# Kernel optimization log

Hardware: AMD Instinct MI355X
Metric: run time of the kernel (lower is better)

## Reference

```python
import jax, jax.numpy as jnp
import numpy as np

B, S, D_IN, D_OUT, H = 2, 2048, 1024, 1024, 16
HD = D_OUT // H


def setup_inputs() -> dict:
    key = jax.random.key(0)
    ks = jax.random.split(key, 6)
    s = 0.02
    return {
        "X": jax.random.normal(ks[0], (B, S, D_IN), dtype=jnp.float32),
        "Wq": jax.random.normal(ks[1], (D_OUT, D_IN), dtype=jnp.float32) * s,
        "Wk": jax.random.normal(ks[2], (D_OUT, D_IN), dtype=jnp.float32) * s,
        "Wv": jax.random.normal(ks[3], (D_OUT, D_IN), dtype=jnp.float32) * s,
        "Wo": jax.random.normal(ks[4], (D_OUT, D_OUT), dtype=jnp.float32) * s,
        "bo": jax.random.normal(ks[5], (D_OUT,), dtype=jnp.float32) * s,
    }


def reference(X, Wq, Wk, Wv, Wo, bo):
    b, n, _ = X.shape
    # torch Linear: y = x @ W^T
    Q = (X @ Wq.T).reshape(b, n, H, HD).transpose(0, 2, 1, 3)  # [b,h,s,hd]
    K = (X @ Wk.T).reshape(b, n, H, HD).transpose(0, 2, 1, 3)
    V = (X @ Wv.T).reshape(b, n, H, HD).transpose(0, 2, 1, 3)
    S_ = jnp.einsum('bhqd,bhkd->bhqk', Q, K)  # [b,h,s,s]
    causal = jnp.triu(jnp.ones((n, n), dtype=bool), k=1)
    S_ = jnp.where(causal, -jnp.inf, S_)
    W = jax.nn.softmax(S_ / jnp.sqrt(jnp.float32(HD)), axis=-1)
    Z = jnp.einsum('bhqk,bhkd->bhqd', W, V)
    Z = Z.transpose(0, 2, 1, 3).reshape(b, n, D_OUT)
    return Z @ Wo.T + bo
```

## Files before the change

kernel.cpp:

```cpp
#include <hip/hip_runtime.h>
#include <stdint.h>

typedef __bf16 bf16x8 __attribute__((ext_vector_type(8)));
typedef float  f32x4  __attribute__((ext_vector_type(4)));

#define S_   2048
#define DM   1024
#define QSCALE 0.18033688011112042f

__device__ __forceinline__ unsigned short f2b(float f) {
    uint32_t u = __builtin_bit_cast(uint32_t, f);
    u += 0x7fffu + ((u >> 16) & 1u);
    return (unsigned short)(u >> 16);
}

__device__ __forceinline__ uint32_t pack2bf(float a, float b) {
    uint32_t ua = __builtin_bit_cast(uint32_t, a) + 0x8000u;
    uint32_t ub = __builtin_bit_cast(uint32_t, b) + 0x8000u;
    return __builtin_amdgcn_perm(ub, ua, 0x07060302);
}

__device__ __forceinline__ void glds16(const void* g, void* l) {
    __builtin_amdgcn_global_load_lds(
        (const __attribute__((address_space(1))) void*)g,
        (__attribute__((address_space(3))) void*)l, 16, 0, 0);
}

__global__ void cvt_all(const float* __restrict__ X,
                        const float* __restrict__ Wq, const float* __restrict__ Wk,
                        const float* __restrict__ Wv,
                        unsigned short* __restrict__ Xb, unsigned short* __restrict__ Wb)
{
    size_t i = ((size_t)blockIdx.x * 256 + threadIdx.x) * 4;
    const float* src;
    unsigned short* dst;
    size_t off;
    if (i < (size_t)4194304) { src = X; dst = Xb; off = i; }
    else {
        size_t j = i - 4194304;
        int sel = (int)(j >> 20);
        off = j & 1048575;
        src = (sel == 0) ? Wq : (sel == 1) ? Wk : Wv;
        dst = Wb + (size_t)sel * 1048576;
    }
    float4 v = *(const float4*)&src[off];
    uint2 o;
    o.x = pack2bf(v.x, v.y);
    o.y = pack2bf(v.z, v.w);
    *(uint2*)&dst[off] = o;
}

__global__ void cvt_wo(const float* __restrict__ Wo, unsigned short* __restrict__ Wob)
{
    size_t i = ((size_t)blockIdx.x * 256 + threadIdx.x) * 4;
    float4 v = *(const float4*)&Wo[i];
    uint2 o;
    o.x = pack2bf(v.x, v.y);
    o.y = pack2bf(v.z, v.w);
    *(uint2*)&Wob[i] = o;
}

__global__ __launch_bounds__(256, 2)
void qkv_gemm(const unsigned short* __restrict__ Xb,
              const unsigned short* __restrict__ Wqb,
              const unsigned short* __restrict__ Wkb,
              const unsigned short* __restrict__ Wvb,
              unsigned short* __restrict__ Qo, unsigned short* __restrict__ Ko,
              unsigned short* __restrict__ Vto)
{
    __shared__ unsigned short Ash[128 * 32];
    __shared__ unsigned short Bsh[128 * 32];

    const int t = threadIdx.x;
    const int lane = t & 63, w = t >> 6;
    const int lcol = lane & 15, quad = lane >> 4;
    const int z = blockIdx.z;
    const int rowBase = ((z == 2) ? blockIdx.x : blockIdx.y) * 128;
    const int colBase = ((z == 2) ? blockIdx.y : blockIdx.x) * 128;
    const unsigned short* aPtr = (z == 2) ? Wvb : Xb;
    const unsigned short* bPtr = (z == 0) ? Wqb : (z == 1) ? Wkb : Xb;
    const int wr = (w >> 1) * 64, wc = (w & 1) * 64;

    f32x4 acc[4][4];
    #pragma unroll
    for (int i = 0; i < 4; ++i)
        #pragma unroll
        for (int j = 0; j < 4; ++j) acc[i][j] = (f32x4){0.f,0.f,0.f,0.f};

    for (int k0 = 0; k0 < DM; k0 += 32) {
        __syncthreads();
        #pragma unroll
        for (int p = 0; p < 2; ++p) {
            int ci = p * 256 + t;
            glds16(&aPtr[(size_t)(rowBase + (ci >> 2)) * DM + k0 + (ci & 3) * 8], &Ash[ci * 8]);
        }
        #pragma unroll
        for (int p = 0; p < 2; ++p) {
            int ci = p * 256 + t;
            glds16(&bPtr[(size_t)(colBase + (ci >> 2)) * DM + k0 + (ci & 3) * 8], &Bsh[ci * 8]);
        }
        __syncthreads();
        bf16x8 af[4], bfr[4];
        #pragma unroll
        for (int i = 0; i < 4; ++i) af[i]  = *(const bf16x8*)&Ash[(wr + i*16 + lcol)*32 + quad*8];
        #pragma unroll
        for (int i = 0; i < 4; ++i) bfr[i] = *(const bf16x8*)&Bsh[(wc + i*16 + lcol)*32 + quad*8];
        #pragma unroll
        for (int i = 0; i < 4; ++i)
            #pragma unroll
            for (int j = 0; j < 4; ++j)
                acc[i][j] = __builtin_amdgcn_mfma_f32_16x16x32_bf16(af[i], bfr[j], acc[i][j], 0, 0, 0);
    }

    unsigned short* Cm = (z == 0) ? Qo : (z == 1) ? Ko : Vto;
    const int ld = (z == 2) ? (S_ * 2) : DM;
    const float sc = (z == 0) ? QSCALE : 1.0f;
    #pragma unroll
    for (int i = 0; i < 4; ++i)
        #pragma unroll
        for (int j = 0; j < 4; ++j)
            #pragma unroll
            for (int r = 0; r < 4; ++r) {
                int row = rowBase + wr + i*16 + quad*4 + r;
                int col = colBase + wc + j*16 + lcol;
                Cm[(size_t)row * ld + col] = f2b(acc[i][j][r] * sc);
            }
}

__global__ __launch_bounds__(512, 8)
void attn_kernel(const unsigned short* __restrict__ Q,
                 const unsigned short* __restrict__ K,
                 const unsigned short* __restrict__ Vt,
                 unsigned short* __restrict__ Z)
{
    __shared__ unsigned short Ks[64 * 72];
    __shared__ unsigned short Vts[64 * 72];
    __shared__ unsigned short Ps[128 * 72];

    const int t = threadIdx.x;
    const int lane = t & 63, w = t >> 6;
    const int lcol = lane & 15, quad = lane >> 4;

    const int bh = blockIdx.x;
    const int b = bh >> 4, h = bh & 15;
    const int y = blockIdx.y;
    const int tile = (y < 8) ? (15 - y) : (y - 8);
    const int q0 = tile * 128;
    const int nchunk = 2 * tile + 2;

    const unsigned short* Qg = Q + (size_t)(b * S_ + q0) * DM + h * 64;
    const unsigned short* Kg = K + (size_t)(b * S_) * DM + h * 64;
    const unsigned short* Vg = Vt + (size_t)(h * 64) * (S_ * 2) + b * S_;

    bf16x8 qf[2];
    #pragma unroll
    for (int kd = 0; kd < 2; ++kd)
        qf[kd] = *(const bf16x8*)&Qg[(size_t)(w*16 + lcol) * DM + kd*32 + quad*8];

    bool mk[4];
    #pragma unroll
    for (int r = 0; r < 4; ++r) mk[r] = (quad*4 + r) > lcol;

    float lpart = 0.f;
    f32x4 o[4];
    #pragma unroll
    for (int nd = 0; nd < 4; ++nd) o[nd] = (f32x4){0.f,0.f,0.f,0.f};

    const int sr = t >> 3, sch = t & 7;

    for (int c = 0; c < nchunk; ++c) {
        const int kc = c * 64;
        __syncthreads();
        *(uint4*)&Ks[sr * 72 + sch * 8] =
            *(const uint4*)&Kg[(size_t)(kc + sr) * DM + sch * 8];
        *(uint4*)&Vts[sr * 72 + sch * 8] =
            *(const uint4*)&Vg[(size_t)sr * (S_ * 2) + kc + sch * 8];
        __syncthreads();

        const int m = tile * 8 + w - c * 4;
        const int nkmax = (m >= 3) ? 4 : (m + 1);
        const int kdmax = (nkmax + 1) >> 1;

        #pragma unroll
        for (int nk = 0; nk < 4; ++nk) {
            if (nk < nkmax) {
                f32x4 s = (f32x4){0.f,0.f,0.f,0.f};
                bf16x8 ak0 = *(const bf16x8*)&Ks[(nk*16 + lcol)*72 + quad*8];
                s = __builtin_amdgcn_mfma_f32_16x16x32_bf16(ak0, qf[0], s, 0, 0, 0);
                bf16x8 ak1 = *(const bf16x8*)&Ks[(nk*16 + lcol)*72 + 32 + quad*8];
                s = __builtin_amdgcn_mfma_f32_16x16x32_bf16(ak1, qf[1], s, 0, 0, 0);
                float p0 = __builtin_amdgcn_exp2f(s[0]);
                float p1 = __builtin_amdgcn_exp2f(s[1]);
                float p2 = __builtin_amdgcn_exp2f(s[2]);
                float p3 = __builtin_amdgcn_exp2f(s[3]);
                if (nk == m) {
                    p0 = mk[0] ? 0.f : p0;
                    p1 = mk[1] ? 0.f : p1;
                    p2 = mk[2] ? 0.f : p2;
                    p3 = mk[3] ? 0.f : p3;
                }
                lpart += (p0 + p1) + (p2 + p3);
                uint2 pk;
                pk.x = pack2bf(p0, p1);
                pk.y = pack2bf(p2, p3);
                *(uint2*)&Ps[(w*16 + lcol) * 72 + nk*16 + quad*4] = pk;
            } else if (nk < 2*kdmax) {
                *(uint2*)&Ps[(w*16 + lcol) * 72 + nk*16 + quad*4] = (uint2){0u, 0u};
            }
        }

        #pragma unroll
        for (int kd2 = 0; kd2 < 2; ++kd2) {
            if (kd2 < kdmax) {
                bf16x8 ap = *(const bf16x8*)&Ps[(w*16 + lcol) * 72 + kd2*32 + quad*8];
                #pragma unroll
                for (int nd = 0; nd < 4; ++nd) {
                    bf16x8 bv = *(const bf16x8*)&Vts[(nd*16 + lcol) * 72 + kd2*32 + quad*8];
                    o[nd] = __builtin_amdgcn_mfma_f32_16x16x32_bf16(ap, bv, o[nd], 0, 0, 0);
                }
            }
        }
    }

    lpart += __shfl_xor(lpart, 16);
    lpart += __shfl_xor(lpart, 32);
    float linv = 1.0f / lpart;
    #pragma unroll
    for (int r = 0; r < 4; ++r) {
        float lr = __shfl(linv, quad*4 + r);
        unsigned short* Zr = Z + (size_t)(b*S_ + q0 + w*16 + quad*4 + r) * DM + h*64;
        #pragma unroll
        for (int nd = 0; nd < 4; ++nd)
            Zr[nd*16 + lcol] = f2b(o[nd][r] * lr);
    }
}

__global__ __launch_bounds__(256, 4)
void out_gemm(const unsigned short* __restrict__ A,
              const unsigned short* __restrict__ Wob, const float* __restrict__ bo,
              float* __restrict__ Out)
{
    __shared__ unsigned short Ash[64 * 32];
    __shared__ unsigned short Bsh[128 * 32];

    const int t = threadIdx.x;
    const int lane = t & 63, w = t >> 6;
    const int lcol = lane & 15, quad = lane >> 4;
    const int rowBase = blockIdx.y * 64;
    const int colBase = blockIdx.x * 128;
    const int wr = (w >> 1) * 32, wc = (w & 1) * 64;

    f32x4 acc[2][4];
    #pragma unroll
    for (int i = 0; i < 2; ++i)
        #pragma unroll
        for (int j = 0; j < 4; ++j) acc[i][j] = (f32x4){0.f,0.f,0.f,0.f};

    for (int k0 = 0; k0 < DM; k0 += 32) {
        __syncthreads();
        glds16(&A[(size_t)(rowBase + (t >> 2)) * DM + k0 + (t & 3) * 8], &Ash[t * 8]);
        #pragma unroll
        for (int p = 0; p < 2; ++p) {
            int ci = p * 256 + t;
            glds16(&Wob[(size_t)(colBase + (ci >> 2)) * DM + k0 + (ci & 3) * 8], &Bsh[ci * 8]);
        }
        __syncthreads();
        bf16x8 af[2], bfr[4];
        #pragma unroll
        for (int i = 0; i < 2; ++i) af[i]  = *(const bf16x8*)&Ash[(wr + i*16 + lcol)*32 + quad*8];
        #pragma unroll
        for (int j = 0; j < 4; ++j) bfr[j] = *(const bf16x8*)&Bsh[(wc + j*16 + lcol)*32 + quad*8];
        #pragma unroll
        for (int i = 0; i < 2; ++i)
            #pragma unroll
            for (int j = 0; j < 4; ++j)
                acc[i][j] = __builtin_amdgcn_mfma_f32_16x16x32_bf16(af[i], bfr[j], acc[i][j], 0, 0, 0);
    }

    float bb[4];
    #pragma unroll
    for (int j = 0; j < 4; ++j) bb[j] = bo[colBase + wc + j*16 + lcol];

    #pragma unroll
    for (int i = 0; i < 2; ++i)
        #pragma unroll
        for (int j = 0; j < 4; ++j)
            #pragma unroll
            for (int r = 0; r < 4; ++r) {
                int row = rowBase + wr + i*16 + quad*4 + r;
                int col = colBase + wc + j*16 + lcol;
                Out[(size_t)row * DM + col] = acc[i][j][r] + bb[j];
            }
}

extern "C" void kernel_launch(void* const* d_in, const int* in_sizes, int n_in,
                              void* d_out, int out_size, void* d_ws, size_t ws_size,
                              hipStream_t stream) {
    const float* X  = (const float*)d_in[0];
    const float* Wq = (const float*)d_in[1];
    const float* Wk = (const float*)d_in[2];
    const float* Wv = (const float*)d_in[3];
    const float* Wo = (const float*)d_in[4];
    const float* bo = (const float*)d_in[5];
    float* out = (float*)d_out;

    unsigned short* Xb  = (unsigned short*)d_ws;
    unsigned short* Qw  = Xb + (size_t)4096 * 1024;
    unsigned short* Kw  = Qw + (size_t)4096 * 1024;
    unsigned short* Vtw = Kw + (size_t)4096 * 1024;
    unsigned short* Zb  = Xb;
    unsigned short* Wob = Qw;
    unsigned short* Wb  = (unsigned short*)d_out;

    cvt_all<<<dim3(7168), 256, 0, stream>>>(X, Wq, Wk, Wv, Xb, Wb);
    qkv_gemm<<<dim3(8, 32, 3), 256, 0, stream>>>(Xb, Wb, Wb + (size_t)1048576,
                                                 Wb + (size_t)2097152, Qw, Kw, Vtw);
    attn_kernel<<<dim3(32, 16), 512, 0, stream>>>(Qw, Kw, Vtw, Zb);
    cvt_wo<<<dim3(1024), 256, 0, stream>>>(Wo, Wob);
    out_gemm<<<dim3(8, 64), 256, 0, stream>>>(Zb, Wob, bo, out);
}
```

Baseline: 185.2 us.

## Double-buffer K/V tiles in attention with register prefetch

Adds a second LDS buffer for the K and V^T chunks. The next chunk is loaded into registers at the start of each iteration and written to the other buffer after compute, so global load latency overlaps the QK/PV MFMA work and one barrier per iteration is dropped. This raises LDS usage and register pressure, and the occupancy hint in launch_bounds is lowered from 8 to 4 blocks.

```diff
diff --git a/kernel.cpp b/kernel.cpp
--- a/kernel.cpp
+++ b/kernel.cpp
@@ -127,14 +127,14 @@
             }
 }
 
-__global__ __launch_bounds__(512, 8)
+__global__ __launch_bounds__(512, 4)
 void attn_kernel(const unsigned short* __restrict__ Q,
                  const unsigned short* __restrict__ K,
                  const unsigned short* __restrict__ Vt,
                  unsigned short* __restrict__ Z)
 {
-    __shared__ unsigned short Ks[64 * 72];
-    __shared__ unsigned short Vts[64 * 72];
+    __shared__ unsigned short Ks[2][64 * 72];
+    __shared__ unsigned short Vts[2][64 * 72];
     __shared__ unsigned short Ps[128 * 72];
 
     const int t = threadIdx.x;
@@ -168,14 +168,26 @@
 
     const int sr = t >> 3, sch = t & 7;
 
+    {
+        uint4 k0 = *(const uint4*)&Kg[(size_t)sr * DM + sch * 8];
+        uint4 v0 = *(const uint4*)&Vg[(size_t)sr * (S_ * 2) + sch * 8];
+        *(uint4*)&Ks[0][sr * 72 + sch * 8] = k0;
+        *(uint4*)&Vts[0][sr * 72 + sch * 8] = v0;
+    }
+    __syncthreads();
+
     for (int c = 0; c < nchunk; ++c) {
-        const int kc = c * 64;
-        __syncthreads();
-        *(uint4*)&Ks[sr * 72 + sch * 8] =
-            *(const uint4*)&Kg[(size_t)(kc + sr) * DM + sch * 8];
-        *(uint4*)&Vts[sr * 72 + sch * 8] =
-            *(const uint4*)&Vg[(size_t)sr * (S_ * 2) + kc + sch * 8];
-        __syncthreads();
+        const int cur = c & 1;
+        const bool pf = (c + 1 < nchunk);
+        uint4 kn, vn;
+        if (pf) {
+            const int kc1 = (c + 1) * 64;
+            kn = *(const uint4*)&Kg[(size_t)(kc1 + sr) * DM + sch * 8];
+            vn = *(const uint4*)&Vg[(size_t)sr * (S_ * 2) + kc1 + sch * 8];
+        }
+
+        const unsigned short* Kc = Ks[cur];
+        const unsigned short* Vc = Vts[cur];
 
         const int m = tile * 8 + w - c * 4;
         const int nkmax = (m >= 3) ? 4 : (m + 1);
@@ -185,9 +197,9 @@
         for (int nk = 0; nk < 4; ++nk) {
             if (nk < nkmax) {
                 f32x4 s = (f32x4){0.f,0.f,0.f,0.f};
-                bf16x8 ak0 = *(const bf16x8*)&Ks[(nk*16 + lcol)*72 + quad*8];
+                bf16x8 ak0 = *(const bf16x8*)&Kc[(nk*16 + lcol)*72 + quad*8];
                 s = __builtin_amdgcn_mfma_f32_16x16x32_bf16(ak0, qf[0], s, 0, 0, 0);
-                bf16x8 ak1 = *(const bf16x8*)&Ks[(nk*16 + lcol)*72 + 32 + quad*8];
+                bf16x8 ak1 = *(const bf16x8*)&Kc[(nk*16 + lcol)*72 + 32 + quad*8];
                 s = __builtin_amdgcn_mfma_f32_16x16x32_bf16(ak1, qf[1], s, 0, 0, 0);
                 float p0 = __builtin_amdgcn_exp2f(s[0]);
                 float p1 = __builtin_amdgcn_exp2f(s[1]);
@@ -215,11 +227,17 @@
                 bf16x8 ap = *(const bf16x8*)&Ps[(w*16 + lcol) * 72 + kd2*32 + quad*8];
                 #pragma unroll
                 for (int nd = 0; nd < 4; ++nd) {
-                    bf16x8 bv = *(const bf16x8*)&Vts[(nd*16 + lcol) * 72 + kd2*32 + quad*8];
+                    bf16x8 bv = *(const bf16x8*)&Vc[(nd*16 + lcol) * 72 + kd2*32 + quad*8];
                     o[nd] = __builtin_amdgcn_mfma_f32_16x16x32_bf16(ap, bv, o[nd], 0, 0, 0);
                 }
             }
         }
+
+        if (pf) {
+            *(uint4*)&Ks[cur ^ 1][sr * 72 + sch * 8] = kn;
+            *(uint4*)&Vts[cur ^ 1][sr * 72 + sch * 8] = vn;
+        }
+        __syncthreads();
     }
 
     lpart += __shfl_xor(lpart, 16);
```

Result: no change. 184.9 us (-0.2%).

## Shrink attention query tile to 64 rows and fuse Wo conversion into output GEMM

Applied to the files above, without the earlier changes.

The attention kernel now uses 64-query tiles with 256 threads (4 waves) instead of 128-query tiles with 512 threads. That doubles the grid, makes causal work balance more finely, and halves the P shared buffer. Each thread loads two K/V chunks per iteration. The separate Wo fp32-to-bf16 conversion kernel is removed: out_gemm reads fp32 Wo directly and packs it to bf16 into shared memory, saving one launch and one round trip through memory. The cost is that each out_gemm block re-reads and re-converts its fp32 Wo tiles, so the Wo traffic is twice as large per load, and K/V is reloaded more often across the smaller attention tiles.

```diff
diff --git a/kernel.cpp b/kernel.cpp
--- a/kernel.cpp
+++ b/kernel.cpp
@@ -50,16 +50,6 @@
     *(uint2*)&dst[off] = o;
 }
 
-__global__ void cvt_wo(const float* __restrict__ Wo, unsigned short* __restrict__ Wob)
-{
-    size_t i = ((size_t)blockIdx.x * 256 + threadIdx.x) * 4;
-    float4 v = *(const float4*)&Wo[i];
-    uint2 o;
-    o.x = pack2bf(v.x, v.y);
-    o.y = pack2bf(v.z, v.w);
-    *(uint2*)&Wob[i] = o;
-}
-
 __global__ __launch_bounds__(256, 2)
 void qkv_gemm(const unsigned short* __restrict__ Xb,
               const unsigned short* __restrict__ Wqb,
@@ -127,7 +117,7 @@
             }
 }
 
-__global__ __launch_bounds__(512, 8)
+__global__ __launch_bounds__(256, 8)
 void attn_kernel(const unsigned short* __restrict__ Q,
                  const unsigned short* __restrict__ K,
                  const unsigned short* __restrict__ Vt,
@@ -135,7 +125,7 @@
 {
     __shared__ unsigned short Ks[64 * 72];
     __shared__ unsigned short Vts[64 * 72];
-    __shared__ unsigned short Ps[128 * 72];
+    __shared__ unsigned short Ps[64 * 72];
 
     const int t = threadIdx.x;
     const int lane = t & 63, w = t >> 6;
@@ -144,9 +134,9 @@
     const int bh = blockIdx.x;
     const int b = bh >> 4, h = bh & 15;
     const int y = blockIdx.y;
-    const int tile = (y < 8) ? (15 - y) : (y - 8);
-    const int q0 = tile * 128;
-    const int nchunk = 2 * tile + 2;
+    const int tile = (y < 16) ? (31 - y) : (y - 16);
+    const int q0 = tile * 64;
+    const int nchunk = tile + 1;
 
     const unsigned short* Qg = Q + (size_t)(b * S_ + q0) * DM + h * 64;
     const unsigned short* Kg = K + (size_t)(b * S_) * DM + h * 64;
@@ -166,18 +156,20 @@
     #pragma unroll
     for (int nd = 0; nd < 4; ++nd) o[nd] = (f32x4){0.f,0.f,0.f,0.f};
 
-    const int sr = t >> 3, sch = t & 7;
-
     for (int c = 0; c < nchunk; ++c) {
         const int kc = c * 64;
         __syncthreads();
-        *(uint4*)&Ks[sr * 72 + sch * 8] =
-            *(const uint4*)&Kg[(size_t)(kc + sr) * DM + sch * 8];
-        *(uint4*)&Vts[sr * 72 + sch * 8] =
-            *(const uint4*)&Vg[(size_t)sr * (S_ * 2) + kc + sch * 8];
-        __syncthreads();
-
-        const int m = tile * 8 + w - c * 4;
+        #pragma unroll
+        for (int p = 0; p < 2; ++p) {
+            int ci = p * 256 + t;
+            *(uint4*)&Ks[(ci >> 3) * 72 + (ci & 7) * 8] =
+                *(const uint4*)&Kg[(size_t)(kc + (ci >> 3)) * DM + (ci & 7) * 8];
+            *(uint4*)&Vts[(ci >> 3) * 72 + (ci & 7) * 8] =
+                *(const uint4*)&Vg[(size_t)(ci >> 3) * (S_ * 2) + kc + (ci & 7) * 8];
+        }
+        __syncthreads();
+
+        const int m = 4 * (tile - c) + w;
         const int nkmax = (m >= 3) ? 4 : (m + 1);
         const int kdmax = (nkmax + 1) >> 1;
 
@@ -237,7 +229,7 @@
 
 __global__ __launch_bounds__(256, 4)
 void out_gemm(const unsigned short* __restrict__ A,
-              const unsigned short* __restrict__ Wob, const float* __restrict__ bo,
+              const float* __restrict__ Wo, const float* __restrict__ bo,
               float* __restrict__ Out)
 {
     __shared__ unsigned short Ash[64 * 32];
@@ -259,10 +251,19 @@
     for (int k0 = 0; k0 < DM; k0 += 32) {
         __syncthreads();
         glds16(&A[(size_t)(rowBase + (t >> 2)) * DM + k0 + (t & 3) * 8], &Ash[t * 8]);
-        #pragma unroll
-        for (int p = 0; p < 2; ++p) {
-            int ci = p * 256 + t;
-            glds16(&Wob[(size_t)(colBase + (ci >> 2)) * DM + k0 + (ci & 3) * 8], &Bsh[ci * 8]);
+        {
+            const float* sb = Wo + (size_t)(colBase + (t >> 1)) * DM + k0 + (t & 1) * 16;
+            float4 v0 = ((const float4*)sb)[0];
+            float4 v1 = ((const float4*)sb)[1];
+            float4 v2 = ((const float4*)sb)[2];
+            float4 v3 = ((const float4*)sb)[3];
+            uint4 tb0, tb1;
+            tb0.x = pack2bf(v0.x, v0.y); tb0.y = pack2bf(v0.z, v0.w);
+            tb0.z = pack2bf(v1.x, v1.y); tb0.w = pack2bf(v1.z, v1.w);
+            tb1.x = pack2bf(v2.x, v2.y); tb1.y = pack2bf(v2.z, v2.w);
+            tb1.z = pack2bf(v3.x, v3.y); tb1.w = pack2bf(v3.z, v3.w);
+            ((uint4*)&Bsh[(t >> 1) * 32 + (t & 1) * 16])[0] = tb0;
+            ((uint4*)&Bsh[(t >> 1) * 32 + (t & 1) * 16])[1] = tb1;
         }
         __syncthreads();
         bf16x8 af[2], bfr[4];
@@ -309,13 +310,11 @@
     unsigned short* Kw  = Qw + (size_t)4096 * 1024;
     unsigned short* Vtw = Kw + (size_t)4096 * 1024;
     unsigned short* Zb  = Xb;
-    unsigned short* Wob = Qw;
     unsigned short* Wb  = (unsigned short*)d_out;
 
     cvt_all<<<dim3(7168), 256, 0, stream>>>(X, Wq, Wk, Wv, Xb, Wb);
     qkv_gemm<<<dim3(8, 32, 3), 256, 0, stream>>>(Xb, Wb, Wb + (size_t)1048576,
                                                  Wb + (size_t)2097152, Qw, Kw, Vtw);
-    attn_kernel<<<dim3(32, 16), 512, 0, stream>>>(Qw, Kw, Vtw, Zb);
-    cvt_wo<<<dim3(1024), 256, 0, stream>>>(Wo, Wob);
-    out_gemm<<<dim3(8, 64), 256, 0, stream>>>(Zb, Wob, bo, out);
-}
+    attn_kernel<<<dim3(32, 32), 256, 0, stream>>>(Qw, Kw, Vtw, Zb);
+    out_gemm<<<dim3(8, 64), 256, 0, stream>>>(Zb, Wo, bo, out);
+}
```

After: 193.1 us. 4.2% more time.

## Switch attention kernel to 32x32x16 MFMA with 4 waves of 32 query rows

Applied to the files above, without the earlier changes.

Rewrites the causal attention inner loop to use 32x32x16 bf16 MFMA tiles instead of 16x16x32. Each block now runs 4 waves of 256 threads, each owning 32 query rows, with cooperative K/V staging split over two passes. The larger tiles raise MFMA work per LDS fragment load and reduce instruction count. In exchange, per-thread accumulator registers grow and there are fewer waves per block to hide latency.

```diff
diff --git a/kernel.cpp b/kernel.cpp
--- a/kernel.cpp
+++ b/kernel.cpp
@@ -3,6 +3,7 @@
 
 typedef __bf16 bf16x8 __attribute__((ext_vector_type(8)));
 typedef float  f32x4  __attribute__((ext_vector_type(4)));
+typedef float  f32x16 __attribute__((ext_vector_type(16)));
 
 #define S_   2048
 #define DM   1024
@@ -127,7 +128,7 @@
             }
 }
 
-__global__ __launch_bounds__(512, 8)
+__global__ __launch_bounds__(256, 2)
 void attn_kernel(const unsigned short* __restrict__ Q,
                  const unsigned short* __restrict__ K,
                  const unsigned short* __restrict__ Vt,
@@ -139,7 +140,7 @@
 
     const int t = threadIdx.x;
     const int lane = t & 63, w = t >> 6;
-    const int lcol = lane & 15, quad = lane >> 4;
+    const int l32 = lane & 31, hi = lane >> 5;
 
     const int bh = blockIdx.x;
     const int b = bh >> 4, h = bh & 15;
@@ -152,87 +153,102 @@
     const unsigned short* Kg = K + (size_t)(b * S_) * DM + h * 64;
     const unsigned short* Vg = Vt + (size_t)(h * 64) * (S_ * 2) + b * S_;
 
-    bf16x8 qf[2];
-    #pragma unroll
-    for (int kd = 0; kd < 2; ++kd)
-        qf[kd] = *(const bf16x8*)&Qg[(size_t)(w*16 + lcol) * DM + kd*32 + quad*8];
-
-    bool mk[4];
-    #pragma unroll
-    for (int r = 0; r < 4; ++r) mk[r] = (quad*4 + r) > lcol;
+    bf16x8 qf[4];
+    #pragma unroll
+    for (int kd = 0; kd < 4; ++kd)
+        qf[kd] = *(const bf16x8*)&Qg[(size_t)(w*32 + l32) * DM + kd*16 + hi*8];
+
+    bool mk[16];
+    #pragma unroll
+    for (int reg = 0; reg < 16; ++reg)
+        mk[reg] = ((reg & 3) + 8 * (reg >> 2) + 4 * hi) > l32;
 
     float lpart = 0.f;
-    f32x4 o[4];
-    #pragma unroll
-    for (int nd = 0; nd < 4; ++nd) o[nd] = (f32x4){0.f,0.f,0.f,0.f};
-
-    const int sr = t >> 3, sch = t & 7;
+    f32x16 o[2];
+    #pragma unroll
+    for (int dblk = 0; dblk < 2; ++dblk)
+        #pragma unroll
+        for (int reg = 0; reg < 16; ++reg) o[dblk][reg] = 0.f;
 
     for (int c = 0; c < nchunk; ++c) {
         const int kc = c * 64;
         __syncthreads();
-        *(uint4*)&Ks[sr * 72 + sch * 8] =
-            *(const uint4*)&Kg[(size_t)(kc + sr) * DM + sch * 8];
-        *(uint4*)&Vts[sr * 72 + sch * 8] =
-            *(const uint4*)&Vg[(size_t)sr * (S_ * 2) + kc + sch * 8];
-        __syncthreads();
-
-        const int m = tile * 8 + w - c * 4;
-        const int nkmax = (m >= 3) ? 4 : (m + 1);
-        const int kdmax = (nkmax + 1) >> 1;
-
-        #pragma unroll
-        for (int nk = 0; nk < 4; ++nk) {
-            if (nk < nkmax) {
-                f32x4 s = (f32x4){0.f,0.f,0.f,0.f};
-                bf16x8 ak0 = *(const bf16x8*)&Ks[(nk*16 + lcol)*72 + quad*8];
-                s = __builtin_amdgcn_mfma_f32_16x16x32_bf16(ak0, qf[0], s, 0, 0, 0);
-                bf16x8 ak1 = *(const bf16x8*)&Ks[(nk*16 + lcol)*72 + 32 + quad*8];
-                s = __builtin_amdgcn_mfma_f32_16x16x32_bf16(ak1, qf[1], s, 0, 0, 0);
-                float p0 = __builtin_amdgcn_exp2f(s[0]);
-                float p1 = __builtin_amdgcn_exp2f(s[1]);
-                float p2 = __builtin_amdgcn_exp2f(s[2]);
-                float p3 = __builtin_amdgcn_exp2f(s[3]);
-                if (nk == m) {
-                    p0 = mk[0] ? 0.f : p0;
-                    p1 = mk[1] ? 0.f : p1;
-                    p2 = mk[2] ? 0.f : p2;
-                    p3 = mk[3] ? 0.f : p3;
-                }
-                lpart += (p0 + p1) + (p2 + p3);
-                uint2 pk;
-                pk.x = pack2bf(p0, p1);
-                pk.y = pack2bf(p2, p3);
-                *(uint2*)&Ps[(w*16 + lcol) * 72 + nk*16 + quad*4] = pk;
-            } else if (nk < 2*kdmax) {
-                *(uint2*)&Ps[(w*16 + lcol) * 72 + nk*16 + quad*4] = (uint2){0u, 0u};
-            }
-        }
-
-        #pragma unroll
-        for (int kd2 = 0; kd2 < 2; ++kd2) {
-            if (kd2 < kdmax) {
-                bf16x8 ap = *(const bf16x8*)&Ps[(w*16 + lcol) * 72 + kd2*32 + quad*8];
-                #pragma unroll
-                for (int nd = 0; nd < 4; ++nd) {
-                    bf16x8 bv = *(const bf16x8*)&Vts[(nd*16 + lcol) * 72 + kd2*32 + quad*8];
-                    o[nd] = __builtin_amdgcn_mfma_f32_16x16x32_bf16(ap, bv, o[nd], 0, 0, 0);
+        #pragma unroll
+        for (int p = 0; p < 2; ++p) {
+            int ci = p * 256 + t;
+            *(uint4*)&Ks[(ci >> 3) * 72 + (ci & 7) * 8] =
+                *(const uint4*)&Kg[(size_t)(kc + (ci >> 3)) * DM + (ci & 7) * 8];
+            *(uint4*)&Vts[(ci >> 3) * 72 + (ci & 7) * 8] =
+                *(const uint4*)&Vg[(size_t)(ci >> 3) * (S_ * 2) + kc + (ci & 7) * 8];
+        }
+        __syncthreads();
+
+        const int M = 4 * tile + w - 2 * c;
+        const int nk2max = (M >= 1) ? 2 : (M + 1);
+        if (nk2max > 0) {
+            #pragma unroll
+            for (int nk2 = 0; nk2 < 2; ++nk2) {
+                if (nk2 < nk2max) {
+                    f32x16 st;
+                    #pragma unroll
+                    for (int reg = 0; reg < 16; ++reg) st[reg] = 0.f;
+                    #pragma unroll
+                    for (int kd = 0; kd < 4; ++kd) {
+                        bf16x8 ak = *(const bf16x8*)&Ks[(nk2*32 + l32)*72 + kd*16 + hi*8];
+                        st = __builtin_amdgcn_mfma_f32_32x32x16_bf16(ak, qf[kd], st, 0, 0, 0);
+                    }
+                    const bool dg = (nk2 == M);
+                    #pragma unroll
+                    for (int g = 0; g < 4; ++g) {
+                        float p0 = __builtin_amdgcn_exp2f(st[4*g + 0]);
+                        float p1 = __builtin_amdgcn_exp2f(st[4*g + 1]);
+                        float p2 = __builtin_amdgcn_exp2f(st[4*g + 2]);
+                        float p3 = __builtin_amdgcn_exp2f(st[4*g + 3]);
+                        if (dg) {
+                            p0 = mk[4*g + 0] ? 0.f : p0;
+                            p1 = mk[4*g + 1] ? 0.f : p1;
+                            p2 = mk[4*g + 2] ? 0.f : p2;
+                            p3 = mk[4*g + 3] ? 0.f : p3;
+                        }
+                        lpart += (p0 + p1) + (p2 + p3);
+                        uint2 pk;
+                        pk.x = pack2bf(p0, p1);
+                        pk.y = pack2bf(p2, p3);
+                        *(uint2*)&Ps[(w*32 + l32) * 72 + nk2*32 + 8*g + 4*hi] = pk;
+                    }
                 }
             }
+
+            const int kbmax = 2 * nk2max;
+            #pragma unroll
+            for (int kb = 0; kb < 4; ++kb) {
+                if (kb < kbmax) {
+                    bf16x8 ap = *(const bf16x8*)&Ps[(w*32 + l32) * 72 + kb*16 + hi*8];
+                    #pragma unroll
+                    for (int dblk = 0; dblk < 2; ++dblk) {
+                        bf16x8 bv = *(const bf16x8*)&Vts[(dblk*32 + l32) * 72 + kb*16 + hi*8];
+                        o[dblk] = __builtin_amdgcn_mfma_f32_32x32x16_bf16(ap, bv, o[dblk], 0, 0, 0);
+                    }
+                }
+            }
         }
     }
 
-    lpart += __shfl_xor(lpart, 16);
     lpart += __shfl_xor(lpart, 32);
     float linv = 1.0f / lpart;
-    #pragma unroll
-    for (int r = 0; r < 4; ++r) {
-        float lr = __shfl(linv, quad*4 + r);
-        unsigned short* Zr = Z + (size_t)(b*S_ + q0 + w*16 + quad*4 + r) * DM + h*64;
-        #pragma unroll
-        for (int nd = 0; nd < 4; ++nd)
-            Zr[nd*16 + lcol] = f2b(o[nd][r] * lr);
-    }
+    float lr[16];
+    #pragma unroll
+    for (int reg = 0; reg < 16; ++reg)
+        lr[reg] = __shfl(linv, (reg & 3) + 8 * (reg >> 2) + 4 * hi);
+
+    #pragma unroll
+    for (int dblk = 0; dblk < 2; ++dblk)
+        #pragma unroll
+        for (int reg = 0; reg < 16; ++reg) {
+            int qrow = (reg & 3) + 8 * (reg >> 2) + 4 * hi;
+            Z[(size_t)(b*S_ + q0 + w*32 + qrow) * DM + h*64 + dblk*32 + l32] =
+                f2b(o[dblk][reg] * lr[reg]);
+        }
 }
 
 __global__ __launch_bounds__(256, 4)
@@ -315,7 +331,7 @@
     cvt_all<<<dim3(7168), 256, 0, stream>>>(X, Wq, Wk, Wv, Xb, Wb);
     qkv_gemm<<<dim3(8, 32, 3), 256, 0, stream>>>(Xb, Wb, Wb + (size_t)1048576,
                                                  Wb + (size_t)2097152, Qw, Kw, Vtw);
-    attn_kernel<<<dim3(32, 16), 512, 0, stream>>>(Qw, Kw, Vtw, Zb);
+    attn_kernel<<<dim3(32, 16), 256, 0, stream>>>(Qw, Kw, Vtw, Zb);
     cvt_wo<<<dim3(1024), 256, 0, stream>>>(Wo, Wob);
     out_gemm<<<dim3(8, 64), 256, 0, stream>>>(Zb, Wob, bo, out);
 }
```

After: 186.6 us. Within noise of the previous version (+0.7%).
